# Kernel optimization log

Hardware: AMD Instinct MI355X
Metric: run time of the kernel (lower is better)

The kernel has to match this reference:

```python
import jax, jax.numpy as jnp
import numpy as np

B, N, C, H = 2, 2048, 1024, 16
D = C // H  # head dim = 64
SCALE = 1.0 / np.sqrt(D)
BASE = 10000.0  # ntk_factor=1.0 => base unchanged


def setup_inputs() -> dict:
    key = jax.random.key(0)
    k1, k2, k3, k4 = jax.random.split(key, 4)
    x = jax.random.normal(k1, (B, N, C), dtype=jnp.float32)
    Wqkv = jax.random.normal(k2, (C, 3 * C), dtype=jnp.float32) * (1.0 / np.sqrt(C))
    Wout = jax.random.normal(k3, (C, C), dtype=jnp.float32) * (1.0 / np.sqrt(C))
    bout = jax.random.normal(k4, (C,), dtype=jnp.float32) * 0.01
    return {"x": x, "Wqkv": Wqkv, "Wout": Wout, "bout": bout}


def _rope_tables(n, d, dtype):
    inv_freq = 1.0 / (BASE ** (jnp.arange(0, d, 2, dtype=jnp.float32) / d))
    t = jnp.arange(n, dtype=jnp.float32)
    freqs = t[:, None] * inv_freq[None, :]            # [N, D/2]
    cos = jnp.cos(freqs)[None, :, None, :].astype(dtype)  # [1,N,1,D/2]
    sin = jnp.sin(freqs)[None, :, None, :].astype(dtype)
    return cos, sin


def _apply_rope(u, cos, sin):
    # u: [B,N,H,D]; strided-halves RoPE variant (cat, not interleave)
    u1, u2 = u[..., ::2], u[..., 1::2]
    return jnp.concatenate([u1 * cos - u2 * sin, u1 * sin + u2 * cos], axis=-1)


def reference(x, Wqkv, Wout, bout):
    b, n, c = x.shape
    qkv = (x @ Wqkv).reshape(b, n, 3, H, D)
    q, k, v = qkv[:, :, 0], qkv[:, :, 1], qkv[:, :, 2]  # [B,N,H,D]
    cos, sin = _rope_tables(n, D, x.dtype)
    q = _apply_rope(q, cos, sin)
    k = _apply_rope(k, cos, sin)
    scores = jnp.einsum("bqhd,bkhd->bhqk", q, k) * SCALE
    causal = jnp.triu(jnp.ones((n, n), dtype=bool), k=1)
    scores = jnp.where(causal, -jnp.inf, scores)
    attn = jax.nn.softmax(scores, axis=-1)
    out = jnp.einsum("bhqk,bkhd->bqhd", attn, v).reshape(b, n, c)
    return out @ Wout + bout
```

## Files before the change

### kernel.cpp

```cpp
#include <hip/hip_runtime.h>
#include <hip/hip_bf16.h>
#include <math.h>

#define B_ 2
#define N_ 2048
#define C_ 1024
#define H_ 16
#define D_ 64
#define M_ 4096
#define QKV_N 3072
#define SCALE_ 0.125f
#define FIXM 8.0f
#define L2E 1.442695041f

typedef unsigned short u16;
typedef unsigned int u32;
using bf16x8   = __attribute__((ext_vector_type(8))) __bf16;
using ushortx8 = __attribute__((ext_vector_type(8))) unsigned short;
using floatx4  = __attribute__((ext_vector_type(4))) float;
using u32x4    = __attribute__((ext_vector_type(4))) u32;

__device__ __forceinline__ float bf2f(u16 u) {
    union { u32 i; float f; } v; v.i = ((u32)u) << 16; return v.f;
}
__device__ __forceinline__ u16 f2bf(float f) {
    union { float f; u32 i; } v; v.f = f;
    u32 r = (v.i + 0x7fff + ((v.i >> 16) & 1)) >> 16;
    return (u16)r;
}
__device__ __forceinline__ u32 pk2bf(float a, float b) {
    __hip_bfloat162 h = __float22bfloat162_rn(make_float2(a, b));
    union { __hip_bfloat162 h; u32 u; } c; c.h = h; return c.u;
}

__device__ __forceinline__ void gl2lds16(const void* g, void* l) {
    __builtin_amdgcn_global_load_lds(
        (const __attribute__((address_space(1))) unsigned int*)(unsigned long long)g,
        (__attribute__((address_space(3))) unsigned int*)(unsigned long long)l,
        16, 0, 0);
}

__constant__ unsigned char UQI[40] = {3,7,7,10,11,11,11,14,14,15,15,15,15,6,6,9,9,10,10,12,12,13,13,13,13,14,14,2,5,5,8,8,8,9,12,12,4,4,1,0};
__constant__ unsigned char UT0[40] = {0,0,8,0,0,8,16,0,8,0,8,16,24,0,7,0,7,8,15,0,7,0,7,14,21,16,23,0,0,6,0,6,12,14,14,20,0,5,0,0};
__constant__ unsigned char UNT[40] = {8,8,8,8,8,8,8,8,8,8,8,8,8,7,7,7,7,7,7,7,7,7,7,7,7,7,7,6,6,6,6,6,6,6,6,6,5,5,4,2};
__constant__ unsigned char UCID[40] = {0,0,1,0,0,1,2,0,1,0,1,2,3,0,1,0,1,1,2,0,1,0,1,2,3,2,3,0,0,1,0,1,2,2,2,3,0,1,0,0};
__constant__ unsigned char CCNT[12] = {2,2,2,2,3,3,3,3,4,4,4,4};
__constant__ unsigned char SOFF[12] = {0,2,4,6,8,11,14,17,20,24,28,32};

__device__ __forceinline__ void do_convtrans(const float* W, u16* Wt, int K, int N,
                                             int nb, int kb, int tid) {
    int n = nb * 256 + tid;
    int k0 = kb * 128;
    #pragma unroll
    for (int kk = 0; kk < 128; kk += 8) {
        ushortx8 v;
        #pragma unroll
        for (int j = 0; j < 8; j++)
            v[j] = f2bf(W[(size_t)(k0 + kk + j) * N + n]);
        *(ushortx8*)(&Wt[(size_t)n * K + k0 + kk]) = v;
    }
}

__global__ __launch_bounds__(256) void prep_kernel(
    const float* __restrict__ x, const float* __restrict__ Wqkv,
    float* __restrict__ cosT, float* __restrict__ sinT,
    u16* __restrict__ xb, u16* __restrict__ Wqkvt)
{
    int bid = blockIdx.x, tid = threadIdx.x;
    if (bid < 2048) {
        int i = bid * 256 + tid;
        const float4* p = (const float4*)x + (size_t)i * 2;
        float4 a = p[0], b = p[1];
        ushortx8 v;
        v[0] = f2bf(a.x); v[1] = f2bf(a.y); v[2] = f2bf(a.z); v[3] = f2bf(a.w);
        v[4] = f2bf(b.x); v[5] = f2bf(b.y); v[6] = f2bf(b.z); v[7] = f2bf(b.w);
        *(ushortx8*)(xb + (size_t)i * 8) = v;
    } else if (bid < 2304) {
        int idx = (bid - 2048) * 256 + tid;
        int n = idx >> 5, i = idx & 31;
        double inv = pow(10000.0, -(double)i / 32.0);
        double f = (double)n * inv;
        cosT[idx] = (float)cos(f);
        sinT[idx] = (float)sin(f);
    } else {
        int u = bid - 2304;
        do_convtrans(Wqkv, Wqkvt, C_, QKV_N, u % 12, u / 12, tid);
    }
}

__global__ __launch_bounds__(256) void gemm128(
    const u16* __restrict__ A, const u16* __restrict__ Bt,
    void* __restrict__ Cm, const float* __restrict__ bias, int fp32out,
    u16* __restrict__ Vt,
    int M, int N, int K)
{
    __shared__ u16 As[128 * 32];
    __shared__ u16 Bs[128 * 32];
    const int t = threadIdx.x;
    const int w = t >> 6, lane = t & 63;
    const int quad = lane >> 4, cc = lane & 15;
    const int m0 = blockIdx.y * 128, n0 = blockIdx.x * 128;
    const int wm = (w >> 1) * 64, wn = (w & 1) * 64;

    floatx4 acc[4][4];
    floatx4 zero = {0.f, 0.f, 0.f, 0.f};
    #pragma unroll
    for (int i = 0; i < 4; i++)
        #pragma unroll
        for (int j = 0; j < 4; j++) acc[i][j] = zero;

    const int srow = lane >> 2, skof = (lane & 3) * 8;

    for (int k0 = 0; k0 < K; k0 += 32) {
        __syncthreads();
        #pragma unroll
        for (int c = 0; c < 2; c++) {
            int chunk = w * 2 + c;
            int row = chunk * 16 + srow;
            gl2lds16(A  + (size_t)(m0 + row) * K + k0 + skof, (char*)As + chunk * 1024);
            gl2lds16(Bt + (size_t)(n0 + row) * K + k0 + skof, (char*)Bs + chunk * 1024);
        }
        __syncthreads();

        bf16x8 af[4], bf[4];
        #pragma unroll
        for (int i = 0; i < 4; i++)
            af[i] = *(const bf16x8*)(&As[(wm + i * 16 + cc) * 32 + quad * 8]);
        #pragma unroll
        for (int j = 0; j < 4; j++)
            bf[j] = *(const bf16x8*)(&Bs[(wn + j * 16 + cc) * 32 + quad * 8]);
        #pragma unroll
        for (int i = 0; i < 4; i++)
            #pragma unroll
            for (int j = 0; j < 4; j++)
                acc[i][j] = __builtin_amdgcn_mfma_f32_16x16x32_bf16(af[i], bf[j], acc[i][j], 0, 0, 0);
    }

    if (Vt && n0 >= 2048) {
        #pragma unroll
        for (int i = 0; i < 4; i++)
            #pragma unroll
            for (int j = 0; j < 4; j++)
                #pragma unroll
                for (int r = 0; r < 4; r++) {
                    int row = m0 + wm + i * 16 + quad * 4 + r;
                    int col2 = n0 + wn + j * 16 + cc - 2048;
                    int h = col2 >> 6, d = col2 & 63;
                    int b = row >> 11, n = row & 2047;
                    int nl = n & 63;
                    size_t idx = (size_t)(b * H_ + h) * (N_ * D_) + (size_t)(n >> 6) * 4096
                               + (size_t)(((nl >> 5) * 4 + ((nl >> 2) & 3)) * 64 + d) * 8
                               + ((nl >> 4) & 1) * 4 + (nl & 3);
                    Vt[idx] = f2bf(acc[i][j][r]);
                }
        return;
    }

    #pragma unroll
    for (int i = 0; i < 4; i++)
        #pragma unroll
        for (int j = 0; j < 4; j++)
            #pragma unroll
            for (int r = 0; r < 4; r++) {
                int row = m0 + wm + i * 16 + quad * 4 + r;
                int col = n0 + wn + j * 16 + cc;
                float v = acc[i][j][r];
                if (fp32out) ((float*)Cm)[(size_t)row * N + col] = v + bias[col];
                else         ((u16*)Cm)[(size_t)row * N + col] = f2bf(v);
            }
}

__global__ void rope_kernel(const u16* __restrict__ qkv,
                            const float* __restrict__ cosT, const float* __restrict__ sinT,
                            u16* __restrict__ Qh, u16* __restrict__ Kh)
{
    int idx = blockIdx.x * 256 + threadIdx.x;
    if (idx >= B_ * N_ * H_ * 32) return;
    int i = idx & 31;
    int h = (idx >> 5) & (H_ - 1);
    int n = (idx >> 9) & (N_ - 1);
    int b = idx >> 20;
    size_t m = (size_t)b * N_ + n;
    const u16* row = qkv + m * QKV_N;
    float cs = cosT[n * 32 + i], sn = sinT[n * 32 + i];

    float q1 = bf2f(row[h * 64 + 2 * i]),      q2 = bf2f(row[h * 64 + 2 * i + 1]);
    float k1 = bf2f(row[C_ + h * 64 + 2 * i]), k2 = bf2f(row[C_ + h * 64 + 2 * i + 1]);
    size_t obase = ((size_t)(b * H_ + h) * N_ + n) * D_;
    Qh[obase + i]      = f2bf((q1 * cs - q2 * sn) * SCALE_);
    Qh[obase + 32 + i] = f2bf((q1 * sn + q2 * cs) * SCALE_);
    Kh[obase + i]      = f2bf(k1 * cs - k2 * sn);
    Kh[obase + 32 + i] = f2bf(k1 * sn + k2 * cs);
}

__global__ __launch_bounds__(256, 3) void attn_kernel(
    const u16* __restrict__ Qh, const u16* __restrict__ Kh,
    const u16* __restrict__ Vt, u16* __restrict__ Ao,
    u16* __restrict__ Opart, float* __restrict__ lpart)
{
    __shared__ u16 Ks[2][64 * 64];
    __shared__ u16 Vs[2][64 * 64];

    const int t = threadIdx.x;
    const int wave = t >> 6, lane = t & 63;
    const int quad = lane >> 4, cc = lane & 15;

    int id = blockIdx.x + 40 * blockIdx.y;
    int e8 = id & 7, s = id >> 3;
    const int u = s % 40;
    const int bh = e8 + 8 * (s / 40);

    const int qi = UQI[u], tile0 = UT0[u], ntl = UNT[u], cid = UCID[u];
    const int qb0 = qi * 128;
    const size_t hb = (size_t)bh * N_ * D_;
    const int qlocal = wave * 16 + cc;

    const int r8 = lane >> 3, sl = lane & 7;
    const int swz = (sl ^ r8) * 8;

    auto STAGE = [&](int kb, int c) {
        #pragma unroll
        for (int i = 0; i < 2; i++) {
            int shot = wave * 2 + i;
            int row = shot * 8 + r8;
            gl2lds16(Kh + hb + (size_t)(kb + row) * 64 + swz, (char*)Ks[c] + shot * 1024);
            gl2lds16(Vt + hb + (size_t)kb * 64 + (size_t)row * 64 + swz, (char*)Vs[c] + shot * 1024);
        }
    };

    bf16x8 qf[2][2];
    #pragma unroll
    for (int qt = 0; qt < 2; qt++) {
        const u16* qrow = Qh + hb + (size_t)(qb0 + qt * 64 + wave * 16 + cc) * D_;
        qf[qt][0] = *(const bf16x8*)(qrow + quad * 8);
        qf[qt][1] = *(const bf16x8*)(qrow + 32 + quad * 8);
    }

    const u32x4 onesw = {0x3F803F80u, 0x3F803F80u, 0x3F803F80u, 0x3F803F80u};
    const bf16x8 ones8 = __builtin_bit_cast(bf16x8, onesw);

    floatx4 zero = {0.f, 0.f, 0.f, 0.f};
    floatx4 Oacc[2][4];
    floatx4 Osum[2];
    #pragma unroll
    for (int qt = 0; qt < 2; qt++) {
        Osum[qt] = zero;
        #pragma unroll
        for (int j = 0; j < 4; j++) Oacc[qt][j] = zero;
    }

    STAGE(tile0 * 64, 0);
    __syncthreads();

    for (int ti = 0; ti < ntl; ti++) {
        const int kb = (tile0 + ti) * 64;
        const int c = ti & 1;
        if (ti + 1 < ntl) STAGE(kb + 64, c ^ 1);
        const bool act0 = (kb <= qb0);

        bf16x8 kf[4][2];
        #pragma unroll
        for (int nt = 0; nt < 4; nt++)
            #pragma unroll
            for (int sfr = 0; sfr < 2; sfr++)
                kf[nt][sfr] = *(const bf16x8*)(
                    &Ks[c][(nt * 16 + cc) * 64 + (((sfr * 4 + quad) ^ (cc & 7)) * 8)]);

        u32 pa[2][4][2];

        {
            floatx4 S[4];
            __builtin_amdgcn_s_setprio(1);
            #pragma unroll
            for (int nt = 0; nt < 4; nt++) {
                floatx4 a = zero;
                a = __builtin_amdgcn_mfma_f32_16x16x32_bf16(kf[nt][0], qf[1][0], a, 0, 0, 0);
                a = __builtin_amdgcn_mfma_f32_16x16x32_bf16(kf[nt][1], qf[1][1], a, 0, 0, 0);
                S[nt] = a;
            }
            __builtin_amdgcn_s_setprio(0);
            const bool diag = (kb == qb0 + 64);
            #pragma unroll
            for (int nt = 0; nt < 4; nt++) {
                float p[4];
                #pragma unroll
                for (int r = 0; r < 4; r++) {
                    int key_l = nt * 16 + quad * 4 + r;
                    float ex = exp2f(fmaf(S[nt][r], L2E, -FIXM * L2E));
                    p[r] = (diag && (key_l > qlocal)) ? 0.0f : ex;
                }
                pa[1][nt][0] = pk2bf(p[0], p[1]);
                pa[1][nt][1] = pk2bf(p[2], p[3]);
            }
        }

        if (act0) {
            floatx4 S0[4];
            __builtin_amdgcn_s_setprio(1);
            #pragma unroll
            for (int nt = 0; nt < 4; nt++) {
                floatx4 a = zero;
                a = __builtin_amdgcn_mfma_f32_16x16x32_bf16(kf[nt][0], qf[0][0], a, 0, 0, 0);
                a = __builtin_amdgcn_mfma_f32_16x16x32_bf16(kf[nt][1], qf[0][1], a, 0, 0, 0);
                S0[nt] = a;
            }
            __builtin_amdgcn_s_setprio(0);
            const bool diag = (kb == qb0);
            #pragma unroll
            for (int nt = 0; nt < 4; nt++) {
                float p[4];
                #pragma unroll
                for (int r = 0; r < 4; r++) {
                    int key_l = nt * 16 + quad * 4 + r;
                    float ex = exp2f(fmaf(S0[nt][r], L2E, -FIXM * L2E));
                    p[r] = (diag && (key_l > qlocal)) ? 0.0f : ex;
                }
                pa[0][nt][0] = pk2bf(p[0], p[1]);
                pa[0][nt][1] = pk2bf(p[2], p[3]);
            }
        }

        __builtin_amdgcn_s_setprio(1);
        #pragma unroll
        for (int g = 0; g < 2; g++) {
            u32x4 aa1 = {pa[1][2 * g][0], pa[1][2 * g][1], pa[1][2 * g + 1][0], pa[1][2 * g + 1][1]};
            bf16x8 A1 = __builtin_bit_cast(bf16x8, aa1);
            bf16x8 A0;
            if (act0) {
                u32x4 aa0 = {pa[0][2 * g][0], pa[0][2 * g][1], pa[0][2 * g + 1][0], pa[0][2 * g + 1][1]};
                A0 = __builtin_bit_cast(bf16x8, aa0);
            }
            #pragma unroll
            for (int j = 0; j < 4; j++) {
                int vrow = (g * 4 + quad) * 8 + j * 2 + (cc >> 3);
                bf16x8 v8 = *(const bf16x8*)(
                    &Vs[c][vrow * 64 + (((cc & 7) ^ (vrow & 7)) * 8)]);
                Oacc[1][j] = __builtin_amdgcn_mfma_f32_16x16x32_bf16(A1, v8, Oacc[1][j], 0, 0, 0);
                if (act0)
                    Oacc[0][j] = __builtin_amdgcn_mfma_f32_16x16x32_bf16(A0, v8, Oacc[0][j], 0, 0, 0);
            }
            Osum[1] = __builtin_amdgcn_mfma_f32_16x16x32_bf16(A1, ones8, Osum[1], 0, 0, 0);
            if (act0)
                Osum[0] = __builtin_amdgcn_mfma_f32_16x16x32_bf16(A0, ones8, Osum[0], 0, 0, 0);
        }
        __builtin_amdgcn_s_setprio(0);

        __syncthreads();
    }

    const bool partial = (qi >= 4);
    const int slot = bh * 36 + SOFF[qi - 4] + cid;
    const int b = bh >> 4, h = bh & (H_ - 1);

    #pragma unroll
    for (int qt = 0; qt < 2; qt++) {
        if (!partial) {
            #pragma unroll
            for (int r = 0; r < 4; r++) {
                float inv = 1.0f / Osum[qt][r];
                int n = qb0 + qt * 64 + wave * 16 + quad * 4 + r;
                #pragma unroll
                for (int j = 0; j < 4; j++)
                    Ao[((size_t)b * N_ + n) * C_ + h * D_ + j * 16 + cc] = f2bf(Oacc[qt][j][r] * inv);
            }
        } else {
            #pragma unroll
            for (int r = 0; r < 4; r++) {
                int lrow = qt * 64 + wave * 16 + quad * 4 + r;
                u16* Ob = Opart + (size_t)slot * (128 * 64) + (size_t)lrow * 64;
                #pragma unroll
                for (int j = 0; j < 4; j++)
                    Ob[j * 16 + cc] = f2bf(Oacc[qt][j][r]);
            }
            if (cc == 0) {
                #pragma unroll
                for (int r = 0; r < 4; r++)
                    lpart[slot * 128 + qt * 64 + wave * 16 + quad * 4 + r] = Osum[qt][r];
            }
        }
    }
}

__global__ __launch_bounds__(256) void attn_combine(
    const u16* __restrict__ Opart, const float* __restrict__ lpart,
    u16* __restrict__ Ao, const float* __restrict__ Wout, u16* __restrict__ Woutt)
{
    if (blockIdx.x >= 3072) {
        int u = blockIdx.x - 3072;
        do_convtrans(Wout, Woutt, C_, C_, u % 4, u / 4, threadIdx.x);
        return;
    }
    int g = blockIdx.x * 256 + threadIdx.x;
    int f4 = g & 15;
    int row = (g >> 4) & 127;
    int v = g >> 11;
    int qz = v % 12, bh = v / 12;
    int cnt = CCNT[qz];
    int s0 = bh * 36 + SOFF[qz];
    float l = 0.f, a0 = 0.f, a1 = 0.f, a2 = 0.f, a3 = 0.f;
    for (int c2 = 0; c2 < cnt; c2++) {
        l += lpart[(s0 + c2) * 128 + row];
        const u16* O = Opart + (size_t)(s0 + c2) * (128 * 64) + (size_t)row * 64 + f4 * 4;
        ushort4 a = *(const ushort4*)O;
        a0 += bf2f(a.x); a1 += bf2f(a.y); a2 += bf2f(a.z); a3 += bf2f(a.w);
    }
    float inv = 1.0f / l;
    int b = bh >> 4, h = bh & (H_ - 1);
    int n = (qz + 4) * 128 + row;
    u16* d = Ao + ((size_t)b * N_ + n) * C_ + h * D_ + f4 * 4;
    d[0] = f2bf(a0 * inv);
    d[1] = f2bf(a1 * inv);
    d[2] = f2bf(a2 * inv);
    d[3] = f2bf(a3 * inv);
}

extern "C" void kernel_launch(void* const* d_in, const int* in_sizes, int n_in,
                              void* d_out, int out_size, void* d_ws, size_t ws_size,
                              hipStream_t stream)
{
    const float* x    = (const float*)d_in[0];
    const float* Wqkv = (const float*)d_in[1];
    const float* Wout = (const float*)d_in[2];
    const float* bout = (const float*)d_in[3];

    char* p = (char*)d_ws;
    u16* qkv = (u16*)p; p += (size_t)M_ * QKV_N * 2;
    u16* Qh  = (u16*)p; p += (size_t)B_ * H_ * N_ * D_ * 2;
    u16* Kh  = (u16*)p; p += (size_t)B_ * H_ * N_ * D_ * 2;
    u16* Vt  = (u16*)p; p += (size_t)B_ * H_ * N_ * D_ * 2;
    u16* Ao  = (u16*)p; p += (size_t)M_ * C_ * 2;
    float* cosT = (float*)p; p += (size_t)N_ * 32 * 4;
    float* sinT = (float*)p; p += (size_t)N_ * 32 * 4;

    u16* xb    = Ao;
    u16* Wqkvt = Qh;
    u16* Woutt = qkv;
    u16* Opart = (u16*)((char*)qkv + ((size_t)2 << 20));
    float* lpart = (float*)((char*)qkv + ((size_t)21 << 20));

    hipLaunchKernelGGL(prep_kernel, dim3(2400), dim3(256), 0, stream,
                       x, Wqkv, cosT, sinT, xb, Wqkvt);
    hipLaunchKernelGGL(gemm128, dim3(QKV_N / 128, M_ / 128), dim3(256), 0, stream,
                       xb, Wqkvt, qkv, (const float*)nullptr, 0, Vt, M_, QKV_N, C_);
    hipLaunchKernelGGL(rope_kernel, dim3((B_ * N_ * H_ * 32) / 256), dim3(256), 0, stream,
                       qkv, cosT, sinT, Qh, Kh);
    hipLaunchKernelGGL(attn_kernel, dim3(40, B_ * H_), dim3(256), 0, stream,
                       Qh, Kh, Vt, Ao, Opart, lpart);
    hipLaunchKernelGGL(attn_combine, dim3(3072 + 32), dim3(256), 0, stream,
                       Opart, lpart, Ao, Wout, Woutt);
    hipLaunchKernelGGL(gemm128, dim3(C_ / 128, M_ / 128), dim3(256), 0, stream,
                       Ao, Woutt, d_out, bout, 1, (u16*)nullptr, M_, C_, C_);
}
```

Baseline: 220.7 us.

## Fuse RoPE into QKV GEMM epilogue, double-buffer LDS, swizzle block order

Applies RoPE and the Q scaling inside the QKV GEMM epilogue, using a lane shuffle to pair even and odd columns, and writes Q/K head-major directly. This removes the separate rope kernel and the round trip of the full qkv buffer through memory. The GEMM main loop now double-buffers the LDS tiles so the next k-slice loads while MFMAs run, which removes one barrier per iteration. Block IDs are swizzled for L2 locality. The cost is double the LDS use and a more complex epilogue with scattered 2-byte stores, and the workspace aliasing is reshuffled.

New measurement: 201.5 us. -8.7%, faster.

```diff
diff --git a/kernel.cpp b/kernel.cpp
--- a/kernel.cpp
+++ b/kernel.cpp
@@ -91,15 +91,22 @@
 __global__ __launch_bounds__(256) void gemm128(
     const u16* __restrict__ A, const u16* __restrict__ Bt,
     void* __restrict__ Cm, const float* __restrict__ bias, int fp32out,
-    u16* __restrict__ Vt,
+    u16* __restrict__ Qho, u16* __restrict__ Kho, u16* __restrict__ Vt,
+    const float* __restrict__ cosT, const float* __restrict__ sinT,
     int M, int N, int K)
 {
-    __shared__ u16 As[128 * 32];
-    __shared__ u16 Bs[128 * 32];
+    __shared__ u16 As[2][128 * 32];
+    __shared__ u16 Bs[2][128 * 32];
     const int t = threadIdx.x;
     const int w = t >> 6, lane = t & 63;
     const int quad = lane >> 4, cc = lane & 15;
-    const int m0 = blockIdx.y * 128, n0 = blockIdx.x * 128;
+
+    const int nbx = gridDim.x;
+    const int nwg = nbx * gridDim.y;
+    int id = blockIdx.y * nbx + blockIdx.x;
+    int qq = nwg >> 3;
+    int swz = (id & 7) * qq + (id >> 3);
+    const int m0 = (swz / nbx) * 128, n0 = (swz % nbx) * 128;
     const int wm = (w >> 1) * 64, wn = (w & 1) * 64;
 
     floatx4 acc[4][4];
@@ -111,24 +118,34 @@
 
     const int srow = lane >> 2, skof = (lane & 3) * 8;
 
+    #pragma unroll
+    for (int c = 0; c < 2; c++) {
+        int chunk = w * 2 + c;
+        int row = chunk * 16 + srow;
+        gl2lds16(A  + (size_t)(m0 + row) * K + skof, (char*)As[0] + chunk * 1024);
+        gl2lds16(Bt + (size_t)(n0 + row) * K + skof, (char*)Bs[0] + chunk * 1024);
+    }
+
     for (int k0 = 0; k0 < K; k0 += 32) {
+        const int cur = (k0 >> 5) & 1;
         __syncthreads();
-        #pragma unroll
-        for (int c = 0; c < 2; c++) {
-            int chunk = w * 2 + c;
-            int row = chunk * 16 + srow;
-            gl2lds16(A  + (size_t)(m0 + row) * K + k0 + skof, (char*)As + chunk * 1024);
-            gl2lds16(Bt + (size_t)(n0 + row) * K + k0 + skof, (char*)Bs + chunk * 1024);
-        }
-        __syncthreads();
+        if (k0 + 32 < K) {
+            #pragma unroll
+            for (int c = 0; c < 2; c++) {
+                int chunk = w * 2 + c;
+                int row = chunk * 16 + srow;
+                gl2lds16(A  + (size_t)(m0 + row) * K + k0 + 32 + skof, (char*)As[cur ^ 1] + chunk * 1024);
+                gl2lds16(Bt + (size_t)(n0 + row) * K + k0 + 32 + skof, (char*)Bs[cur ^ 1] + chunk * 1024);
+            }
+        }
 
         bf16x8 af[4], bf[4];
         #pragma unroll
         for (int i = 0; i < 4; i++)
-            af[i] = *(const bf16x8*)(&As[(wm + i * 16 + cc) * 32 + quad * 8]);
+            af[i] = *(const bf16x8*)(&As[cur][(wm + i * 16 + cc) * 32 + quad * 8]);
         #pragma unroll
         for (int j = 0; j < 4; j++)
-            bf[j] = *(const bf16x8*)(&Bs[(wn + j * 16 + cc) * 32 + quad * 8]);
+            bf[j] = *(const bf16x8*)(&Bs[cur][(wn + j * 16 + cc) * 32 + quad * 8]);
         #pragma unroll
         for (int i = 0; i < 4; i++)
             #pragma unroll
@@ -136,23 +153,51 @@
                 acc[i][j] = __builtin_amdgcn_mfma_f32_16x16x32_bf16(af[i], bf[j], acc[i][j], 0, 0, 0);
     }
 
-    if (Vt && n0 >= 2048) {
-        #pragma unroll
-        for (int i = 0; i < 4; i++)
-            #pragma unroll
-            for (int j = 0; j < 4; j++)
-                #pragma unroll
-                for (int r = 0; r < 4; r++) {
-                    int row = m0 + wm + i * 16 + quad * 4 + r;
-                    int col2 = n0 + wn + j * 16 + cc - 2048;
-                    int h = col2 >> 6, d = col2 & 63;
-                    int b = row >> 11, n = row & 2047;
-                    int nl = n & 63;
-                    size_t idx = (size_t)(b * H_ + h) * (N_ * D_) + (size_t)(n >> 6) * 4096
-                               + (size_t)(((nl >> 5) * 4 + ((nl >> 2) & 3)) * 64 + d) * 8
-                               + ((nl >> 4) & 1) * 4 + (nl & 3);
-                    Vt[idx] = f2bf(acc[i][j][r]);
+    if (Qho) {
+        if (n0 >= 2048) {
+            #pragma unroll
+            for (int i = 0; i < 4; i++)
+                #pragma unroll
+                for (int j = 0; j < 4; j++)
+                    #pragma unroll
+                    for (int r = 0; r < 4; r++) {
+                        int row = m0 + wm + i * 16 + quad * 4 + r;
+                        int col2 = n0 + wn + j * 16 + cc - 2048;
+                        int h = col2 >> 6, d = col2 & 63;
+                        int b = row >> 11, n = row & 2047;
+                        int nl = n & 63;
+                        size_t idx = (size_t)(b * H_ + h) * (N_ * D_) + (size_t)(n >> 6) * 4096
+                                   + (size_t)(((nl >> 5) * 4 + ((nl >> 2) & 3)) * 64 + d) * 8
+                                   + ((nl >> 4) & 1) * 4 + (nl & 3);
+                        Vt[idx] = f2bf(acc[i][j][r]);
+                    }
+        } else {
+            u16* dst = (n0 < 1024) ? Qho : Kho;
+            const float scale = (n0 < 1024) ? SCALE_ : 1.0f;
+            const bool ev = (cc & 1) == 0;
+            #pragma unroll
+            for (int i = 0; i < 4; i++)
+                #pragma unroll
+                for (int j = 0; j < 4; j++) {
+                    int col = n0 + wn + j * 16 + cc;
+                    int h = (col >> 6) & (H_ - 1);
+                    int ri = (col & 63) >> 1;
+                    #pragma unroll
+                    for (int r = 0; r < 4; r++) {
+                        int row = m0 + wm + i * 16 + quad * 4 + r;
+                        int nn = row & (N_ - 1), bb = row >> 11;
+                        float v = acc[i][j][r];
+                        float pt = __shfl_xor(v, 1, 64);
+                        float cs = cosT[nn * 32 + ri], sn = sinT[nn * 32 + ri];
+                        float u1 = ev ? v : pt;
+                        float u2 = ev ? pt : v;
+                        float o = ev ? (u1 * cs - u2 * sn) : (u1 * sn + u2 * cs);
+                        size_t oi = (size_t)(bb * H_ + h) * (N_ * D_) + (size_t)nn * 64
+                                  + (ev ? ri : 32 + ri);
+                        dst[oi] = f2bf(o * scale);
+                    }
                 }
+        }
         return;
     }
 
@@ -168,29 +213,6 @@
                 if (fp32out) ((float*)Cm)[(size_t)row * N + col] = v + bias[col];
                 else         ((u16*)Cm)[(size_t)row * N + col] = f2bf(v);
             }
-}
-
-__global__ void rope_kernel(const u16* __restrict__ qkv,
-                            const float* __restrict__ cosT, const float* __restrict__ sinT,
-                            u16* __restrict__ Qh, u16* __restrict__ Kh)
-{
-    int idx = blockIdx.x * 256 + threadIdx.x;
-    if (idx >= B_ * N_ * H_ * 32) return;
-    int i = idx & 31;
-    int h = (idx >> 5) & (H_ - 1);
-    int n = (idx >> 9) & (N_ - 1);
-    int b = idx >> 20;
-    size_t m = (size_t)b * N_ + n;
-    const u16* row = qkv + m * QKV_N;
-    float cs = cosT[n * 32 + i], sn = sinT[n * 32 + i];
-
-    float q1 = bf2f(row[h * 64 + 2 * i]),      q2 = bf2f(row[h * 64 + 2 * i + 1]);
-    float k1 = bf2f(row[C_ + h * 64 + 2 * i]), k2 = bf2f(row[C_ + h * 64 + 2 * i + 1]);
-    size_t obase = ((size_t)(b * H_ + h) * N_ + n) * D_;
-    Qh[obase + i]      = f2bf((q1 * cs - q2 * sn) * SCALE_);
-    Qh[obase + 32 + i] = f2bf((q1 * sn + q2 * cs) * SCALE_);
-    Kh[obase + i]      = f2bf(k1 * cs - k2 * sn);
-    Kh[obase + 32 + i] = f2bf(k1 * sn + k2 * cs);
 }
 
 __global__ __launch_bounds__(256, 3) void attn_kernel(
@@ -424,7 +446,7 @@
     const float* bout = (const float*)d_in[3];
 
     char* p = (char*)d_ws;
-    u16* qkv = (u16*)p; p += (size_t)M_ * QKV_N * 2;
+    char* scratch = p;      p += (size_t)M_ * QKV_N * 2;
     u16* Qh  = (u16*)p; p += (size_t)B_ * H_ * N_ * D_ * 2;
     u16* Kh  = (u16*)p; p += (size_t)B_ * H_ * N_ * D_ * 2;
     u16* Vt  = (u16*)p; p += (size_t)B_ * H_ * N_ * D_ * 2;
@@ -433,21 +455,22 @@
     float* sinT = (float*)p; p += (size_t)N_ * 32 * 4;
 
     u16* xb    = Ao;
-    u16* Wqkvt = Qh;
-    u16* Woutt = qkv;
-    u16* Opart = (u16*)((char*)qkv + ((size_t)2 << 20));
-    float* lpart = (float*)((char*)qkv + ((size_t)21 << 20));
+    u16* Woutt = (u16*)scratch;
+    u16* Wqkvt = (u16*)(scratch + ((size_t)2 << 20));
+    u16* Opart = (u16*)(scratch + ((size_t)2 << 20));
+    float* lpart = (float*)(scratch + ((size_t)21 << 20));
 
     hipLaunchKernelGGL(prep_kernel, dim3(2400), dim3(256), 0, stream,
                        x, Wqkv, cosT, sinT, xb, Wqkvt);
     hipLaunchKernelGGL(gemm128, dim3(QKV_N / 128, M_ / 128), dim3(256), 0, stream,
-                       xb, Wqkvt, qkv, (const float*)nullptr, 0, Vt, M_, QKV_N, C_);
-    hipLaunchKernelGGL(rope_kernel, dim3((B_ * N_ * H_ * 32) / 256), dim3(256), 0, stream,
-                       qkv, cosT, sinT, Qh, Kh);
+                       xb, Wqkvt, (void*)nullptr, (const float*)nullptr, 0,
+                       Qh, Kh, Vt, cosT, sinT, M_, QKV_N, C_);
     hipLaunchKernelGGL(attn_kernel, dim3(40, B_ * H_), dim3(256), 0, stream,
                        Qh, Kh, Vt, Ao, Opart, lpart);
     hipLaunchKernelGGL(attn_combine, dim3(3072 + 32), dim3(256), 0, stream,
                        Opart, lpart, Ao, Wout, Woutt);
     hipLaunchKernelGGL(gemm128, dim3(C_ / 128, M_ / 128), dim3(256), 0, stream,
-                       Ao, Woutt, d_out, bout, 1, (u16*)nullptr, M_, C_, C_);
-}
+                       Ao, Woutt, d_out, bout, 1,
+                       (u16*)nullptr, (u16*)nullptr, (u16*)nullptr,
+                       (const float*)nullptr, (const float*)nullptr, M_, C_, C_);
+}
```
